# Optimization experiments

Hardware: AMD Instinct MI355X
Metric: run time of the kernel (lower is better)

Reference implementation:

```python
import jax, jax.numpy as jnp
import numpy as np

NPOINT, RADIUS, NSAMPLE = 1024, 0.4, 32
BN_EPS = 1e-5


def fps(xyz, npoint):
    # xyz: [B, N, 3]. Deterministic start at index 0 (torch uses randint).
    B, N, _ = xyz.shape

    def step(carry, _):
        distance, farthest = carry  # [B,N], [B]
        centroid = jnp.take_along_axis(xyz, farthest[:, None, None], axis=1)  # [B,1,3]
        dist = jnp.sum((xyz - centroid) ** 2, -1)  # [B,N]
        distance = jnp.minimum(distance, dist)
        new_far = jnp.argmax(distance, axis=-1).astype(jnp.int32)
        return (distance, new_far), farthest

    init = (jnp.full((B, N), 1e10, xyz.dtype), jnp.zeros((B,), jnp.int32))
    _, cents = jax.lax.scan(step, init, None, length=npoint)  # [npoint, B]
    return cents.T  # [B, npoint]


def square_distance(src, dst):
    # src [B,S,3], dst [B,N,3] -> [B,S,N]
    d = -2.0 * jnp.einsum('bsc,bnc->bsn', src, dst)
    d = d + jnp.sum(src ** 2, -1)[:, :, None] + jnp.sum(dst ** 2, -1)[:, None, :]
    return jnp.clip(d, 1e-12, None)


def query_ball_point(radius, nsample, xyz, new_xyz):
    B, N, _ = xyz.shape
    S = new_xyz.shape[1]
    sqr = square_distance(new_xyz, xyz)  # [B,S,N]
    gi = jnp.where(sqr > radius ** 2, N, jnp.arange(N, dtype=jnp.int32)[None, None, :])
    gi = jnp.sort(gi, axis=-1)[:, :, :nsample]  # [B,S,K]
    first = gi[:, :, :1]
    return jnp.where(gi == N, first, gi)


def gather_points(points, idx):
    # points [B,N,C], idx [B,S,K] -> [B,S,K,C]
    B, S, K = idx.shape
    C = points.shape[-1]
    flat = jnp.take_along_axis(points, idx.reshape(B, S * K)[:, :, None], axis=1)
    return flat.reshape(B, S, K, C)


def setup_inputs() -> dict:
    key = jax.random.key(0)
    ks = jax.random.split(key, 10)
    B, N, D = 8, 4096, 64
    inp = {
        'xyz': jax.random.normal(ks[0], (B, 3, N), jnp.float32),
        'points': jax.random.normal(ks[1], (B, D, N), jnp.float32),
    }
    chans = [67, 64, 64, 128]
    for i in range(3):
        cin, cout = chans[i], chans[i + 1]
        inp[f'W{i}'] = jax.random.normal(ks[2 + i], (cout, cin), jnp.float32) * (1.0 / np.sqrt(cin))
        inp[f'b{i}'] = jnp.zeros((cout,), jnp.float32)
        inp[f'g{i}'] = jnp.ones((cout,), jnp.float32)
        inp[f'bt{i}'] = jnp.zeros((cout,), jnp.float32)
    return inp


def _forward(xyz, points, Ws, bs, gs, bts):
    xyz_t = jnp.transpose(xyz, (0, 2, 1))      # [B,N,3]
    pts_t = jnp.transpose(points, (0, 2, 1))   # [B,N,D]
    B, N, _ = xyz_t.shape

    fps_idx = fps(xyz_t, NPOINT)                              # [B,S]
    new_xyz = jnp.take_along_axis(xyz_t, fps_idx[:, :, None], axis=1)  # [B,S,3]
    idx = query_ball_point(RADIUS, NSAMPLE, xyz_t, new_xyz)   # [B,S,K]

    grouped_xyz = gather_points(xyz_t, idx)                   # [B,S,K,3]
    grouped_xyz_norm = grouped_xyz - new_xyz[:, :, None, :]
    grouped_pts = gather_points(pts_t, idx)                   # [B,S,K,D]
    new_points = jnp.concatenate([grouped_xyz_norm, grouped_pts], -1)  # [B,S,K,3+D]

    x = jnp.transpose(new_points, (0, 3, 2, 1))  # [B,C,K,S]
    for W, b, g, bt in zip(Ws, bs, gs, bts):
        x = jnp.einsum('oc,bcks->boks', W, x) + b[None, :, None, None]
        mean = jnp.mean(x, axis=(0, 2, 3), keepdims=True)
        var = jnp.var(x, axis=(0, 2, 3), keepdims=True)
        x = (x - mean) * jax.lax.rsqrt(var + BN_EPS)
        x = x * g[None, :, None, None] + bt[None, :, None, None]
        x = jax.nn.relu(x)
    out = jnp.max(x, axis=2)                      # [B,C_out,S]
    return jnp.transpose(new_xyz, (0, 2, 1)), out


def reference(xyz, points, W0, b0, g0, bt0, W1, b1, g1, bt1, W2, b2, g2, bt2):
    return _forward(xyz, points, (W0, W1, W2), (b0, b1, b2), (g0, g1, g2), (bt0, bt1, bt2))
```

## Files before the change

kernel.cpp:

```cpp
#include <hip/hip_runtime.h>
#include <cstddef>
#include <cstdint>

#define NB 8
#define NPTS 4096
#define NS 1024
#define NK 32
#define ND 64

#define DPP_IMAX(v, ctrl)                                                     \
  {                                                                           \
    int _o = __builtin_amdgcn_update_dpp(v, v, ctrl, 0xf, 0xf, false);        \
    v = (_o > v) ? _o : v;                                                    \
  }

#define DPP_FADD(v, ctrl)                                                     \
  {                                                                           \
    int _t = __builtin_amdgcn_update_dpp(__float_as_int(v), __float_as_int(v),\
                                         ctrl, 0xf, 0xf, false);              \
    v = v + __int_as_float(_t);                                               \
  }

__global__ __launch_bounds__(256, 1) void fps_kernel(const float* __restrict__ xyz,
                                                     float* __restrict__ out_newxyz,
                                                     float* __restrict__ ws_newxyz) {
  const int b = blockIdx.x;
  const int t = threadIdx.x;
  const int wave = t >> 6;
  const int lane = t & 63;
  __shared__ float sXYZ[NPTS * 3];
  __shared__ __align__(16) unsigned long long sRed[2][4];
  __shared__ int sWidx[NS];
  const float* xb = xyz + (size_t)b * 3 * NPTS;

  for (int i = t; i < NPTS; i += 256) {
    sXYZ[i * 3 + 0] = xb[i];
    sXYZ[i * 3 + 1] = xb[NPTS + i];
    sXYZ[i * 3 + 2] = xb[2 * NPTS + i];
  }
  if (t == 0) sWidx[0] = 0;

  float px[16], py[16], pz[16], dist[16];
#pragma unroll
  for (int q = 0; q < 4; ++q) {
    float4 a = ((const float4*)xb)[4 * t + q];
    float4 bq = ((const float4*)(xb + NPTS))[4 * t + q];
    float4 c = ((const float4*)(xb + 2 * NPTS))[4 * t + q];
    px[4 * q + 0] = a.x;  px[4 * q + 1] = a.y;  px[4 * q + 2] = a.z;  px[4 * q + 3] = a.w;
    py[4 * q + 0] = bq.x; py[4 * q + 1] = bq.y; py[4 * q + 2] = bq.z; py[4 * q + 3] = bq.w;
    pz[4 * q + 0] = c.x;  pz[4 * q + 1] = c.y;  pz[4 * q + 2] = c.z;  pz[4 * q + 3] = c.w;
  }
#pragma unroll
  for (int j = 0; j < 16; ++j) dist[j] = 1e10f;

  float cx = xb[0], cy = xb[NPTS], cz = xb[2 * NPTS];

  for (int s = 0; s < NS; ++s) {
#pragma unroll
    for (int j = 0; j < 16; ++j) {
      float dx = __fadd_rn(px[j], -cx);
      float dy = __fadd_rn(py[j], -cy);
      float dz = __fadd_rn(pz[j], -cz);
      float d = __fadd_rn(__fadd_rn(__fmul_rn(dx, dx), __fmul_rn(dy, dy)), __fmul_rn(dz, dz));
      dist[j] = fminf(dist[j], d);
    }
    float m0 = fmaxf(fmaxf(fmaxf(dist[0], dist[1]), fmaxf(dist[2], dist[3])),
                     fmaxf(fmaxf(dist[4], dist[5]), fmaxf(dist[6], dist[7])));
    float m1 = fmaxf(fmaxf(fmaxf(dist[8], dist[9]), fmaxf(dist[10], dist[11])),
                     fmaxf(fmaxf(dist[12], dist[13]), fmaxf(dist[14], dist[15])));
    float m = fmaxf(m0, m1);
    int v = __float_as_int(m);
    DPP_IMAX(v, 0x111)
    DPP_IMAX(v, 0x112)
    DPP_IMAX(v, 0x114)
    DPP_IMAX(v, 0x118)
    DPP_IMAX(v, 0x142)
    DPP_IMAX(v, 0x143)
    const int wm_i = __builtin_amdgcn_readlane(v, 63);
    const float wm = __int_as_float(wm_i);
    unsigned long long claim = __ballot(m == wm);
    int firstlane = __ffsll(claim) - 1;
    if (lane == firstlane) {
      int j = 15;
#pragma unroll
      for (int jj = 14; jj >= 0; --jj)
        if (dist[jj] == wm) j = jj;
      unsigned widx = (unsigned)(t * 16 + j);
      sRed[s & 1][wave] = ((unsigned long long)(unsigned)wm_i << 32) |
                          (unsigned long long)(0xFFFFFFFFu - widx);
    }
    __syncthreads();
    ulonglong2 ka = *(const ulonglong2*)&sRed[s & 1][0];
    ulonglong2 kb = *(const ulonglong2*)&sRed[s & 1][2];
    unsigned long long k = ka.x;
    if (ka.y > k) k = ka.y;
    if (kb.x > k) k = kb.x;
    if (kb.y > k) k = kb.y;
    const int widx = (int)(0xFFFFFFFFu - (unsigned)(k & 0xFFFFFFFFull));
    cx = sXYZ[widx * 3 + 0];
    cy = sXYZ[widx * 3 + 1];
    cz = sXYZ[widx * 3 + 2];
    if (t == 0 && s < NS - 1) sWidx[s + 1] = widx;
  }
  __syncthreads();
  for (int s2 = t; s2 < NS; s2 += 256) {
    int w = sWidx[s2];
    float x = sXYZ[w * 3 + 0], y = sXYZ[w * 3 + 1], z = sXYZ[w * 3 + 2];
    out_newxyz[b * 3 * NS + s2] = x;
    out_newxyz[b * 3 * NS + NS + s2] = y;
    out_newxyz[b * 3 * NS + 2 * NS + s2] = z;
    ws_newxyz[((b << 10) + s2) * 3 + 0] = x;
    ws_newxyz[((b << 10) + s2) * 3 + 1] = y;
    ws_newxyz[((b << 10) + s2) * 3 + 2] = z;
  }
}

__global__ __launch_bounds__(256) void query_kernel(const float* __restrict__ xyz,
                                                    const float* __restrict__ ws_newxyz,
                                                    int* __restrict__ idx_ws) {
  const int w = threadIdx.x >> 6;
  const int lane = threadIdx.x & 63;
  const int p = blockIdx.x * 4 + w;
  const int b = p >> 10;
  __shared__ int sIdx[4][32];
  const float* xb = xyz + (size_t)b * 3 * NPTS;
  const float cx = ws_newxyz[p * 3 + 0];
  const float cy = ws_newxyz[p * 3 + 1];
  const float cz = ws_newxyz[p * 3 + 2];
  const float ss = __fadd_rn(__fadd_rn(__fmul_rn(cx, cx), __fmul_rn(cy, cy)), __fmul_rn(cz, cz));
  const float r2 = (float)(0.4 * 0.4);
  int cnt = 0;
  for (int ci = 0; ci < 64 && cnt < 32; ++ci) {
    int n = ci * 64 + lane;
    float x = xb[n], y = xb[NPTS + n], z = xb[2 * NPTS + n];
    float dot = __fadd_rn(__fadd_rn(__fmul_rn(cx, x), __fmul_rn(cy, y)), __fmul_rn(cz, z));
    float dd = __fadd_rn(__fadd_rn(__fmul_rn(x, x), __fmul_rn(y, y)), __fmul_rn(z, z));
    float d = __fmul_rn(-2.0f, dot);
    d = __fadd_rn(d, ss);
    d = __fadd_rn(d, dd);
    d = fmaxf(d, 1e-12f);
    bool inc = (d <= r2);
    unsigned long long m = __ballot(inc);
    int slot = cnt + (int)__popcll(m & ((1ull << lane) - 1ull));
    if (inc && slot < 32) sIdx[w][slot] = n;
    cnt += (int)__popcll(m);
  }
  if (lane < 32) {
    int v;
    if (lane < cnt) v = sIdx[w][lane];
    else v = (cnt > 0) ? sIdx[w][0] : 0;
    idx_ws[p * 32 + lane] = v;
  }
}

__global__ __launch_bounds__(256) void pgemm_kernel(const float* __restrict__ points,
                                                    const float* __restrict__ W0,
                                                    const float* __restrict__ b0,
                                                    float* __restrict__ P1) {
  const int blk = blockIdx.x;
  const int b = blk >> 6;
  const int n0 = (blk & 63) * 64;
  const int t = threadIdx.x;
  __shared__ __align__(16) float sP[64 * 64];
  __shared__ __align__(16) float sW[64 * 68];
  __shared__ float sB[64];
  const float* pb = points + (size_t)b * ND * NPTS;
  for (int f = t; f < 4096; f += 256) {
    int c = f >> 6, n = f & 63;
    sP[f] = pb[c * NPTS + n0 + n];
  }
  for (int f = t; f < 4096; f += 256) {
    int c = f >> 6, o = f & 63;
    sW[c * 68 + o] = W0[o * 67 + 3 + c];
  }
  if (t < 64) sB[t] = b0[t];
  __syncthreads();
  const int nl = (t & 15) * 4;
  const int ol = (t >> 4) * 4;
  float acc[4][4];
#pragma unroll
  for (int i = 0; i < 4; ++i)
#pragma unroll
    for (int j = 0; j < 4; ++j) acc[i][j] = 0.f;
#pragma unroll 4
  for (int c = 0; c < 64; ++c) {
    float4 xv = *(const float4*)(sP + c * 64 + nl);
    float4 wv = *(const float4*)(sW + c * 68 + ol);
    float xa[4] = {xv.x, xv.y, xv.z, xv.w};
    float wa[4] = {wv.x, wv.y, wv.z, wv.w};
#pragma unroll
    for (int i = 0; i < 4; ++i)
#pragma unroll
      for (int j = 0; j < 4; ++j) acc[i][j] += xa[i] * wa[j];
  }
#pragma unroll
  for (int i = 0; i < 4; ++i) {
    float4 v = make_float4(acc[i][0] + sB[ol + 0], acc[i][1] + sB[ol + 1],
                           acc[i][2] + sB[ol + 2], acc[i][3] + sB[ol + 3]);
    *(float4*)(P1 + ((size_t)(b << 12) + n0 + nl + i) * 64 + ol) = v;
  }
}

__global__ __launch_bounds__(256) void gather0_kernel(
    const float* __restrict__ xyz, const float* __restrict__ P1,
    const int* __restrict__ idx_ws, const float* __restrict__ cen_ws,
    const float* __restrict__ W0, float* __restrict__ y0,
    float* __restrict__ partials) {
  const int t = threadIdx.x;
  const int wave = t >> 6, lane = t & 63;
  const int pair0 = blockIdx.x * 2;
  const int b = pair0 >> 10;
  __shared__ int sIdx[64];
  __shared__ float sCen[2 * 4];
  __shared__ float sY[64 * 65];
  __shared__ float sWS[4 * 64];
  __shared__ float sWQ[4 * 64];
  if (t < 64) sIdx[t] = idx_ws[pair0 * 32 + t];
  if (t < 6) sCen[(t / 3) * 4 + (t % 3)] = cen_ws[pair0 * 3 + t];
  const float wx = W0[lane * 67 + 0];
  const float wy = W0[lane * 67 + 1];
  const float wz = W0[lane * 67 + 2];
  __syncthreads();
  const float* xb = xyz + (size_t)b * 3 * NPTS;
  float ssum = 0.f, ssq = 0.f;
  for (int r = wave; r < 64; r += 4) {
    const int sl = r >> 5;
    const int n = sIdx[r];
    float P1v = P1[((size_t)(b << 12) + n) * 64 + lane];
    float dx = __fadd_rn(xb[n], -sCen[sl * 4 + 0]);
    float dy = __fadd_rn(xb[NPTS + n], -sCen[sl * 4 + 1]);
    float dz = __fadd_rn(xb[2 * NPTS + n], -sCen[sl * 4 + 2]);
    float y = P1v + (dx * wx + dy * wy + dz * wz);
    ssum += y;
    ssq += y * y;
    sY[r * 65 + lane] = y;
  }
  sWS[wave * 64 + lane] = ssum;
  sWQ[wave * 64 + lane] = ssq;
  __syncthreads();
  for (int f = t; f < 4096; f += 256) {
    int sl = f >> 11;
    int rmd = f & 2047;
    int o = rmd >> 5, k = rmd & 31;
    y0[(size_t)(pair0 + sl) * 2048 + rmd] = sY[(sl * 32 + k) * 65 + o];
  }
  if (t < 64) {
    float s1 = sWS[t] + sWS[64 + t] + sWS[128 + t] + sWS[192 + t];
    float s2 = sWQ[t] + sWQ[64 + t] + sWQ[128 + t] + sWQ[192 + t];
    partials[(size_t)blockIdx.x * 128 + t] = s1;
    partials[(size_t)blockIdx.x * 128 + 64 + t] = s2;
  }
}

template <int CIN, int COUT, int SPB, int MODE>
__global__ __launch_bounds__(256) void conv_kernel(
    const float* __restrict__ xin, const float* __restrict__ W,
    const float* __restrict__ bias, const float* __restrict__ scaleA,
    const float* __restrict__ shiftA, float* __restrict__ yout,
    float* __restrict__ pmax, float* __restrict__ pmin,
    float* __restrict__ partials) {
  constexpr int WP = COUT + 4;
  constexpr int TPS = (COUT / 4) * 8;
  __shared__ __align__(16) float sW[CIN * WP];
  __shared__ __align__(16) float sX[SPB * CIN * 32];
  __shared__ float sScale[CIN];
  __shared__ float sShift[CIN];
  __shared__ float sSum[COUT];
  __shared__ float sSq[COUT];
  __shared__ float sMax[8 * COUT];
  __shared__ float sMin[8 * COUT];

  const int t = threadIdx.x;
  const int pair0 = blockIdx.x * SPB;

  for (int f = t; f < CIN * COUT; f += 256) {
    int o = f / CIN;
    int c = f - o * CIN;
    sW[c * WP + o] = W[f];
  }
  if (t < CIN) { sScale[t] = scaleA[t]; sShift[t] = shiftA[t]; }
  if (t < COUT) { sSum[t] = 0.f; sSq[t] = 0.f; }
  __syncthreads();

  for (int f = t; f < SPB * CIN * 32; f += 256) {
    int c = (f >> 5) % CIN;
    float v = xin[(size_t)pair0 * CIN * 32 + f];
    v = v * sScale[c] + sShift[c];
    sX[f] = fmaxf(v, 0.f);
  }
  __syncthreads();

  const int sl = t / TPS;
  const int tl = t - sl * TPS;
  const int k0 = (tl & 7) * 4;
  const int o0 = (tl >> 3) * 4;

  float acc[4][4];
#pragma unroll
  for (int i = 0; i < 4; ++i)
#pragma unroll
    for (int j = 0; j < 4; ++j) acc[i][j] = 0.f;

  const float* xrow = sX + sl * (CIN * 32);
#pragma unroll 4
  for (int c = 0; c < CIN; ++c) {
    float4 xv = *(const float4*)(xrow + c * 32 + k0);
    float4 wv = *(const float4*)(sW + c * WP + o0);
    float xa[4] = {xv.x, xv.y, xv.z, xv.w};
    float wa[4] = {wv.x, wv.y, wv.z, wv.w};
#pragma unroll
    for (int i = 0; i < 4; ++i)
#pragma unroll
      for (int j = 0; j < 4; ++j) acc[i][j] += wa[i] * xa[j];
  }
#pragma unroll
  for (int i = 0; i < 4; ++i) {
    float bo = bias[o0 + i];
#pragma unroll
    for (int j = 0; j < 4; ++j) acc[i][j] += bo;
  }
#pragma unroll
  for (int i = 0; i < 4; ++i) {
    float s1 = (acc[i][0] + acc[i][1]) + (acc[i][2] + acc[i][3]);
    float s2 = (acc[i][0] * acc[i][0] + acc[i][1] * acc[i][1]) +
               (acc[i][2] * acc[i][2] + acc[i][3] * acc[i][3]);
    DPP_FADD(s1, 0x111)
    DPP_FADD(s1, 0x112)
    DPP_FADD(s1, 0x114)
    DPP_FADD(s2, 0x111)
    DPP_FADD(s2, 0x112)
    DPP_FADD(s2, 0x114)
    if ((t & 7) == 7) {
      atomicAdd(&sSum[o0 + i], s1);
      atomicAdd(&sSq[o0 + i], s2);
    }
  }
  if (MODE < 2) {
#pragma unroll
    for (int i = 0; i < 4; ++i) {
      float4 v = make_float4(acc[i][0], acc[i][1], acc[i][2], acc[i][3]);
      *(float4*)(yout + (size_t)(pair0 + sl) * COUT * 32 + (o0 + i) * 32 + k0) = v;
    }
  } else {
#pragma unroll
    for (int i = 0; i < 4; ++i) {
      float mx = fmaxf(fmaxf(acc[i][0], acc[i][1]), fmaxf(acc[i][2], acc[i][3]));
      float mn = fminf(fminf(acc[i][0], acc[i][1]), fminf(acc[i][2], acc[i][3]));
      sMax[(k0 >> 2) * COUT + o0 + i] = mx;
      sMin[(k0 >> 2) * COUT + o0 + i] = mn;
    }
  }
  __syncthreads();
  if (t < COUT) {
    partials[(size_t)blockIdx.x * (COUT * 2) + t] = sSum[t];
    partials[(size_t)blockIdx.x * (COUT * 2) + COUT + t] = sSq[t];
    if (MODE == 2) {
      float mx = sMax[t];
      float mn = sMin[t];
#pragma unroll
      for (int q = 1; q < 8; ++q) {
        mx = fmaxf(mx, sMax[q * COUT + t]);
        mn = fminf(mn, sMin[q * COUT + t]);
      }
      pmax[pair0 * COUT + t] = mx;
      pmin[pair0 * COUT + t] = mn;
    }
  }
}

template <int COUT>
__global__ __launch_bounds__(256) void stats_kernel(const float* __restrict__ partials,
                                                    int nblocks,
                                                    const float* __restrict__ gA,
                                                    const float* __restrict__ btA,
                                                    float* __restrict__ scaleA,
                                                    float* __restrict__ shiftA) {
  const int o = blockIdx.x;
  const int t = threadIdx.x;
  double s1 = 0.0, s2 = 0.0;
  for (int blk = t; blk < nblocks; blk += 256) {
    s1 += (double)partials[(size_t)blk * (COUT * 2) + o];
    s2 += (double)partials[(size_t)blk * (COUT * 2) + COUT + o];
  }
  __shared__ double r1[256], r2[256];
  r1[t] = s1; r2[t] = s2;
  __syncthreads();
  for (int st = 128; st > 0; st >>= 1) {
    if (t < st) { r1[t] += r1[t + st]; r2[t] += r2[t + st]; }
    __syncthreads();
  }
  if (t == 0) {
    const double Nr = 262144.0;
    double mean = r1[0] / Nr;
    double var = r2[0] / Nr - mean * mean;
    double rstd = 1.0 / sqrt(var + 1e-5);
    double sc = rstd * (double)gA[o];
    scaleA[o] = (float)sc;
    shiftA[o] = (float)((double)btA[o] - mean * sc);
  }
}

__global__ __launch_bounds__(256) void stats_final_kernel(
    const float* __restrict__ partials, int nblocks,
    const float* __restrict__ pmax, const float* __restrict__ pmin,
    const float* __restrict__ gA, const float* __restrict__ btA,
    float* __restrict__ out) {
  const int o = blockIdx.x;
  const int t = threadIdx.x;
  double s1 = 0.0, s2 = 0.0;
  for (int blk = t; blk < nblocks; blk += 256) {
    s1 += (double)partials[(size_t)blk * 256 + o];
    s2 += (double)partials[(size_t)blk * 256 + 128 + o];
  }
  __shared__ double r1[256], r2[256];
  __shared__ float sMean, sRstd;
  r1[t] = s1; r2[t] = s2;
  __syncthreads();
  for (int st = 128; st > 0; st >>= 1) {
    if (t < st) { r1[t] += r1[t + st]; r2[t] += r2[t + st]; }
    __syncthreads();
  }
  if (t == 0) {
    const double Nr = 262144.0;
    double mean = r1[0] / Nr;
    double var = r2[0] / Nr - mean * mean;
    sMean = (float)mean;
    sRstd = (float)(1.0 / sqrt(var + 1e-5));
  }
  __syncthreads();
  const float mn = sMean, rs = sRstd, gg = gA[o], bb = btA[o];
  const float slope = rs * gg;
  const float* src = (slope >= 0.f) ? pmax : pmin;
  for (int i = t; i < NB * NS; i += 256) {
    int b = i >> 10;
    int s = i & 1023;
    float v = src[(size_t)i * 128 + o];
    float t1 = (v - mn) * rs;
    float t2 = t1 * gg + bb;
    out[(size_t)b * (128 * NS) + o * NS + s] = fmaxf(t2, 0.f);
  }
}

extern "C" void kernel_launch(void* const* d_in, const int* in_sizes, int n_in,
                              void* d_out, int out_size, void* d_ws, size_t ws_size,
                              hipStream_t stream) {
  (void)in_sizes; (void)n_in; (void)out_size; (void)ws_size;
  const float* xyz = (const float*)d_in[0];
  const float* points = (const float*)d_in[1];
  const float* W0 = (const float*)d_in[2];
  const float* b0 = (const float*)d_in[3];
  const float* g0 = (const float*)d_in[4];
  const float* bt0 = (const float*)d_in[5];
  const float* W1 = (const float*)d_in[6];
  const float* b1 = (const float*)d_in[7];
  const float* g1 = (const float*)d_in[8];
  const float* bt1 = (const float*)d_in[9];
  const float* W2 = (const float*)d_in[10];
  const float* b2 = (const float*)d_in[11];
  const float* g2 = (const float*)d_in[12];
  const float* bt2 = (const float*)d_in[13];
  float* out = (float*)d_out;

  float* ws = (float*)d_ws;
  size_t off = 0;
  float* newxyz = ws + off;  off += (size_t)NB * NS * 3;
  int* idx = (int*)(ws + off); off += (size_t)NB * NS * NK;
  float* y0 = ws + off;      off += (size_t)NB * NS * 64 * 32;
  float* y1 = ws + off;      off += (size_t)NB * NS * 64 * 32;
  float* partials = ws + off; off += (size_t)8192 * 256;
  float* scaleA = ws + off;  off += 128;
  float* shiftA = ws + off;  off += 128;
  float* pmaxb = ws + off;   off += (size_t)NB * NS * 128;
  float* pminb = ws + off;   off += (size_t)NB * NS * 128;
  float* P1 = y1;

  fps_kernel<<<NB, 256, 0, stream>>>(xyz, out, newxyz);
  query_kernel<<<2048, 256, 0, stream>>>(xyz, newxyz, idx);
  pgemm_kernel<<<512, 256, 0, stream>>>(points, W0, b0, P1);
  gather0_kernel<<<4096, 256, 0, stream>>>(xyz, P1, idx, newxyz, W0, y0, partials);
  stats_kernel<64><<<64, 256, 0, stream>>>(partials, 4096, g0, bt0, scaleA, shiftA);
  conv_kernel<64, 64, 2, 1><<<4096, 256, 0, stream>>>(
      y0, W1, b1, scaleA, shiftA, y1, nullptr, nullptr, partials);
  stats_kernel<64><<<64, 256, 0, stream>>>(partials, 4096, g1, bt1, scaleA, shiftA);
  conv_kernel<64, 128, 1, 2><<<8192, 256, 0, stream>>>(
      y1, W2, b2, scaleA, shiftA, nullptr, pmaxb, pminb, partials);
  stats_final_kernel<<<128, 256, 0, stream>>>(partials, 8192, pmaxb, pminb,
                                              g2, bt2, out + NB * NS * 3);
}
```

Baseline: 1.053 ms.

## Replace FPS block barrier with LDS flag spin-wait and carry winner coordinates

In the farthest-point-sampling loop, the per-iteration __syncthreads is replaced by per-wave progress tags in shared memory that each wave spins on. Each wave now publishes its local maximum together with the point's coordinates, so the winner's xyz is taken straight from the reduction. This removes the shared-memory xyz staging and the dependent index-to-coordinate lookup on the serial critical path. Centroids are recorded per step in a float4 shared array for the final write-out. The cost is busy-wait polling on volatile LDS and reliance on the double-buffered exchange slots staying race-free.

```diff
diff --git a/kernel.cpp b/kernel.cpp
--- a/kernel.cpp
+++ b/kernel.cpp
@@ -28,17 +28,10 @@
   const int t = threadIdx.x;
   const int wave = t >> 6;
   const int lane = t & 63;
-  __shared__ float sXYZ[NPTS * 3];
-  __shared__ __align__(16) unsigned long long sRed[2][4];
-  __shared__ int sWidx[NS];
+  __shared__ __align__(16) float4 sE[2][4];
+  __shared__ int sTag[4];
+  __shared__ __align__(16) float4 sCent[NS];
   const float* xb = xyz + (size_t)b * 3 * NPTS;
-
-  for (int i = t; i < NPTS; i += 256) {
-    sXYZ[i * 3 + 0] = xb[i];
-    sXYZ[i * 3 + 1] = xb[NPTS + i];
-    sXYZ[i * 3 + 2] = xb[2 * NPTS + i];
-  }
-  if (t == 0) sWidx[0] = 0;
 
   float px[16], py[16], pz[16], dist[16];
 #pragma unroll
@@ -53,9 +46,14 @@
 #pragma unroll
   for (int j = 0; j < 16; ++j) dist[j] = 1e10f;
 
+  if (lane == 0) sTag[wave] = 0;
+  __syncthreads();
+
   float cx = xb[0], cy = xb[NPTS], cz = xb[2 * NPTS];
+  volatile int* vt = (volatile int*)sTag;
 
   for (int s = 0; s < NS; ++s) {
+    if (t == 0) sCent[s] = make_float4(cx, cy, cz, 0.f);
 #pragma unroll
     for (int j = 0; j < 16; ++j) {
       float dx = __fadd_rn(px[j], -cx);
@@ -85,33 +83,30 @@
 #pragma unroll
       for (int jj = 14; jj >= 0; --jj)
         if (dist[jj] == wm) j = jj;
-      unsigned widx = (unsigned)(t * 16 + j);
-      sRed[s & 1][wave] = ((unsigned long long)(unsigned)wm_i << 32) |
-                          (unsigned long long)(0xFFFFFFFFu - widx);
-    }
-    __syncthreads();
-    ulonglong2 ka = *(const ulonglong2*)&sRed[s & 1][0];
-    ulonglong2 kb = *(const ulonglong2*)&sRed[s & 1][2];
-    unsigned long long k = ka.x;
-    if (ka.y > k) k = ka.y;
-    if (kb.x > k) k = kb.x;
-    if (kb.y > k) k = kb.y;
-    const int widx = (int)(0xFFFFFFFFu - (unsigned)(k & 0xFFFFFFFFull));
-    cx = sXYZ[widx * 3 + 0];
-    cy = sXYZ[widx * 3 + 1];
-    cz = sXYZ[widx * 3 + 2];
-    if (t == 0 && s < NS - 1) sWidx[s + 1] = widx;
+      sE[s & 1][wave] = make_float4(wm, px[j], py[j], pz[j]);
+    }
+    __threadfence_block();
+    if (lane == 0) sTag[wave] = s + 1;
+    while (vt[0] < s + 1 || vt[1] < s + 1 || vt[2] < s + 1 || vt[3] < s + 1) {}
+    __threadfence_block();
+    float4 e0 = sE[s & 1][0], e1 = sE[s & 1][1];
+    float4 e2 = sE[s & 1][2], e3 = sE[s & 1][3];
+    float4 a01 = (e1.x > e0.x) ? e1 : e0;
+    float4 a23 = (e3.x > e2.x) ? e3 : e2;
+    float4 w4 = (a23.x > a01.x) ? a23 : a01;
+    cx = w4.y;
+    cy = w4.z;
+    cz = w4.w;
   }
   __syncthreads();
   for (int s2 = t; s2 < NS; s2 += 256) {
-    int w = sWidx[s2];
-    float x = sXYZ[w * 3 + 0], y = sXYZ[w * 3 + 1], z = sXYZ[w * 3 + 2];
-    out_newxyz[b * 3 * NS + s2] = x;
-    out_newxyz[b * 3 * NS + NS + s2] = y;
-    out_newxyz[b * 3 * NS + 2 * NS + s2] = z;
-    ws_newxyz[((b << 10) + s2) * 3 + 0] = x;
-    ws_newxyz[((b << 10) + s2) * 3 + 1] = y;
-    ws_newxyz[((b << 10) + s2) * 3 + 2] = z;
+    float4 c = sCent[s2];
+    out_newxyz[b * 3 * NS + s2] = c.x;
+    out_newxyz[b * 3 * NS + NS + s2] = c.y;
+    out_newxyz[b * 3 * NS + 2 * NS + s2] = c.z;
+    ws_newxyz[((b << 10) + s2) * 3 + 0] = c.x;
+    ws_newxyz[((b << 10) + s2) * 3 + 1] = c.y;
+    ws_newxyz[((b << 10) + s2) * 3 + 2] = c.z;
   }
 }
 
```

Measured after the change: 1.593 ms. +51.2%, slower.
